# Performance work log

Hardware: AMD Instinct MI355X
Metric: run time of the kernel (lower is better)

Reference implementation:

```python
import jax, jax.numpy as jnp
import numpy as np

NBITS = 8
QMAX = 2 ** (NBITS - 1) - 1  # 127
EPS_S = 1e-8


def ste_round(x):
    # straight-through estimator round (matches HAWQ ste_round)
    return x + jax.lax.stop_gradient(jnp.round(x) - x)


def quant_act(x):
    # symmetric per-tensor 8-bit fake quantization (QuantAct)
    s = jnp.maximum(jnp.max(jnp.abs(x)) / QMAX, EPS_S)
    xq = jnp.clip(ste_round(x / s), -QMAX - 1, QMAX)
    return xq * s, s


def quant_weight_per_channel(w, axis=0):
    # symmetric per-output-channel 8-bit fake quantization (weights)
    red = tuple(i for i in range(w.ndim) if i != axis)
    s = jnp.maximum(jnp.max(jnp.abs(w), axis=red, keepdims=True) / QMAX, EPS_S)
    wq = jnp.clip(ste_round(w / s), -QMAX - 1, QMAX)
    return wq * s, s


def setup_inputs() -> dict:
    key = jax.random.key(0)
    ks = jax.random.split(key, 6)
    B, Cin, Cout, H, W = 32, 256, 128, 56, 56
    x = jax.random.normal(ks[0], (B, Cin, H, W), jnp.float32)
    bn_gamma = 1.0 + 0.1 * jax.random.normal(ks[1], (Cin,), jnp.float32)
    bn_beta = 0.1 * jax.random.normal(ks[2], (Cin,), jnp.float32)
    bn_mean = 0.1 * jax.random.normal(ks[3], (Cin,), jnp.float32)
    bn_var = jax.random.uniform(ks[4], (Cin,), jnp.float32, minval=0.5, maxval=1.5)
    conv_w = jax.random.normal(ks[5], (Cout, Cin), jnp.float32) * (1.0 / np.sqrt(Cin))
    return {"x": x, "bn_gamma": bn_gamma, "bn_beta": bn_beta,
            "bn_mean": bn_mean, "bn_var": bn_var, "conv_w": conv_w}


def reference(x, bn_gamma, bn_beta, bn_mean, bn_var, conv_w):
    bn_eps = 1e-5
    # --- QuantAct on incoming activations ---
    x, act_s = quant_act(x)
    # --- QuantBn: fold BN into per-channel scale/shift, quantize folded weight ---
    w_fold = bn_gamma * jax.lax.rsqrt(bn_var + bn_eps)        # [Cin]
    b_fold = bn_beta - bn_mean * w_fold                       # [Cin]
    wq, bn_s = quant_weight_per_channel(w_fold, axis=0)
    x = x * wq[None, :, None, None] + b_fold[None, :, None, None]
    # --- QuantAct1: requantize post-BN output (act_s * bn_s threaded) ---
    x, act_s = quant_act(x)
    # --- ReLU ---
    x = jax.nn.relu(x)
    # --- QuantConv2d: 1x1 conv, per-output-channel quantized weight ---
    cwq, conv_s = quant_weight_per_channel(conv_w, axis=0)    # [Cout, Cin]
    x = jnp.einsum('bchw,oc->bohw', x, cwq)                   # [B, Cout, H, W]
    # --- QuantAct2: requantize post-conv output ---
    x, act_s = quant_act(x)
    # --- QuantAveragePool2d(2,2): pool in integer domain, rescale back ---
    B, C, H, W = x.shape
    x_int = x / act_s
    pooled = x_int.reshape(B, C, H // 2, 2, W // 2, 2).mean(axis=(3, 5))
    x = pooled * act_s
    # --- QuantAct3 ---
    x, act_s = quant_act(x)
    return x, act_s
```

## Files before the change

kernel.cpp:

```cpp
#include <hip/hip_runtime.h>
#include <math.h>

#define QMAXF 127.0f
#define EPSF  1e-8f
#define CIN   256
#define COUT  128
#define HW    3136
#define W_    56
#define NPOOL 3211264
#define POOL_BLOCKS 1792

typedef unsigned short u16;
typedef unsigned int   u32;
typedef __attribute__((ext_vector_type(8))) short s16x8;
typedef __attribute__((ext_vector_type(4))) float f32x4;

#define WQ_OFF   8
#define BF_OFF   264
#define EMAX_OFF 520
#define EMIN_OFF 776
#define CS_OFF   1032
#define CSS2_OFF 1160
#define CWB_OFF  1288
#define LUT_OFF  17672
#define Y_OFF    50440

__device__ __forceinline__ float qclip(float v) {
    return fminf(fmaxf(v, -128.0f), 127.0f);
}
__device__ __forceinline__ u16 bf16bits(float f) {
    return (u16)(__float_as_uint(f) >> 16);
}
__device__ __forceinline__ u32 encf(float f) {
    u32 u = __float_as_uint(f);
    return (u & 0x80000000u) ? ~u : (u | 0x80000000u);
}
__device__ __forceinline__ float decf(u32 k) {
    return __uint_as_float((k & 0x80000000u) ? (k ^ 0x80000000u) : ~k);
}

__device__ __forceinline__ void block_max_atomic(float v, float* red, u32* dst) {
    #pragma unroll
    for (int off = 32; off > 0; off >>= 1) v = fmaxf(v, __shfl_xor(v, off));
    const int lane = threadIdx.x & 63, wid = threadIdx.x >> 6;
    if (lane == 0) red[wid] = v;
    __syncthreads();
    if (threadIdx.x == 0) {
        const int nw = blockDim.x >> 6;
        float m = red[0];
        for (int i = 1; i < nw; ++i) m = fmaxf(m, red[i]);
        atomicMax(dst, __float_as_uint(m));
    }
}

__global__ void k0w(const float* __restrict__ cw, float* __restrict__ ws) {
    const int t = threadIdx.x;
    if (blockIdx.x == COUT) {
        ((u32*)ws)[EMAX_OFF + t] = 0u;
        ((u32*)ws)[EMIN_OFF + t] = 0xFFFFFFFFu;
        if (t < 2) ((u32*)ws)[2 + t] = 0u;
        return;
    }
    __shared__ float red[4];
    const int o = blockIdx.x;
    const float wv = cw[o * CIN + t];
    float v = fabsf(wv);
    #pragma unroll
    for (int off = 32; off > 0; off >>= 1) v = fmaxf(v, __shfl_xor(v, off));
    if ((t & 63) == 0) red[t >> 6] = v;
    __syncthreads();
    const float mx = fmaxf(fmaxf(red[0], red[1]), fmaxf(red[2], red[3]));
    const float s = fmaxf(mx / QMAXF, EPSF);
    const float q = qclip(rintf(wv / s));
    ((u16*)(ws + CWB_OFF))[o * CIN + t] = bf16bits(q);
    if (t == 0) ws[CS_OFF + o] = s;
}

__global__ void k1_minmax(const float* __restrict__ x, float* __restrict__ ws) {
    __shared__ float red[8];
    const int row = blockIdx.x;
    const float4* xr = (const float4*)(x + (size_t)row * HW);
    float mx = -3.402823466e38f, mn = 3.402823466e38f;
    for (int i = threadIdx.x; i < HW / 4; i += 256) {
        const float4 v = xr[i];
        mx = fmaxf(mx, fmaxf(fmaxf(v.x, v.y), fmaxf(v.z, v.w)));
        mn = fminf(mn, fminf(fminf(v.x, v.y), fminf(v.z, v.w)));
    }
    #pragma unroll
    for (int off = 32; off > 0; off >>= 1) {
        mx = fmaxf(mx, __shfl_xor(mx, off));
        mn = fminf(mn, __shfl_xor(mn, off));
    }
    if ((threadIdx.x & 63) == 0) {
        red[threadIdx.x >> 6] = mx;
        red[4 + (threadIdx.x >> 6)] = mn;
    }
    __syncthreads();
    if (threadIdx.x == 0) {
        mx = fmaxf(fmaxf(red[0], red[1]), fmaxf(red[2], red[3]));
        mn = fminf(fminf(red[4], red[5]), fminf(red[6], red[7]));
        const int c = row & (CIN - 1);
        atomicMax((u32*)ws + EMAX_OFF + c, encf(mx));
        atomicMin((u32*)ws + EMIN_OFF + c, encf(mn));
    }
}

__global__ void k0b(const float* __restrict__ g, const float* __restrict__ be,
                    const float* __restrict__ mnp, const float* __restrict__ vr,
                    float* __restrict__ ws) {
    __shared__ float red[4];
    __shared__ float s1sh;
    const int t = threadIdx.x;
    const float cmax = decf(((u32*)ws)[EMAX_OFF + t]);
    const float cmin = decf(((u32*)ws)[EMIN_OFF + t]);
    float v = fmaxf(fabsf(cmax), fabsf(cmin));
    #pragma unroll
    for (int off = 32; off > 0; off >>= 1) v = fmaxf(v, __shfl_xor(v, off));
    if ((t & 63) == 0) red[t >> 6] = v;
    __syncthreads();
    if (t == 0) {
        const float m1 = fmaxf(fmaxf(red[0], red[1]), fmaxf(red[2], red[3]));
        ws[0] = m1;
        s1sh = fmaxf(m1 / QMAXF, EPSF);
    }
    __syncthreads();
    const float s1 = s1sh;
    const float wf = g[t] / sqrtf(vr[t] + 1e-5f);
    const float bf = be[t] - mnp[t] * wf;
    const float sw = fmaxf(fabsf(wf) / QMAXF, EPSF);
    const float q  = qclip(rintf(wf / sw));
    const float wqd = __fmul_rn(q, sw);
    ws[WQ_OFF + t] = wqd;
    ws[BF_OFF + t] = bf;
    const float q1h = qclip(rintf(cmax / s1));
    const float q1l = qclip(rintf(cmin / s1));
    const float xh = __fadd_rn(__fmul_rn(__fmul_rn(q1h, s1), wqd), bf);
    const float xl = __fadd_rn(__fmul_rn(__fmul_rn(q1l, s1), wqd), bf);
    float m2 = fmaxf(fabsf(xh), fabsf(xl));
    __syncthreads();
    #pragma unroll
    for (int off = 32; off > 0; off >>= 1) m2 = fmaxf(m2, __shfl_xor(m2, off));
    if ((t & 63) == 0) red[t >> 6] = m2;
    __syncthreads();
    if (t == 0) ws[1] = fmaxf(fmaxf(red[0], red[1]), fmaxf(red[2], red[3]));
}

__global__ void k0L(float* __restrict__ ws) {
    const int c = blockIdx.x;
    const int t = threadIdx.x;
    const float s1 = fmaxf(ws[0] / QMAXF, EPSF);
    const float s2 = fmaxf(ws[1] / QMAXF, EPSF);
    const float wqd = ws[WQ_OFF + c];
    const float bf  = ws[BF_OFF + c];
    const float q1f = (float)(t - 127);
    const float xd  = __fmul_rn(q1f, s1);
    const float x2  = __fadd_rn(__fmul_rn(xd, wqd), bf);
    const float q2  = qclip(rintf(x2 / s2));
    const float a   = fmaxf(q2, 0.0f);
    ((u16*)(ws + LUT_OFF))[(c << 8) + t] = bf16bits(a);
    if (c == 0 && t < COUT)
        ws[CSS2_OFF + t] = __fmul_rn(s2, ws[CS_OFF + t]);
}

__device__ __forceinline__ void stage32(u16* __restrict__ Xs, u16* __restrict__ Wt,
                                        const float* __restrict__ xr8,
                                        const s16x8* __restrict__ wreg,
                                        int t, int ck, double rinv,
                                        const u16* __restrict__ lut) {
    const int p = t & 31, kh = t >> 5;
    u32 pk[4];
    #pragma unroll
    for (int jj = 0; jj < 4; ++jj) {
        const int c0 = ck + kh * 8 + 2 * jj;
        const int q1a = (int)rintf((float)((double)xr8[2 * jj] * rinv));
        const int q1b = (int)rintf((float)((double)xr8[2 * jj + 1] * rinv));
        const u32 lo = lut[(c0 << 8) + 127 + q1a];
        const u32 hi = lut[((c0 + 1) << 8) + 127 + q1b];
        pk[jj] = lo | (hi << 16);
    }
    uint4 v; v.x = pk[0]; v.y = pk[1]; v.z = pk[2]; v.w = pk[3];
    *(uint4*)&Xs[p * 64 + (((kh + p + (p >> 3)) & 7) * 8)] = v;
    #pragma unroll
    for (int ps = 0; ps < 4; ++ps) {
        const int o = ps * 32 + (t >> 3);
        *(s16x8*)&Wt[o * 64 + ((((t & 7) + o + (o >> 3)) & 7) * 8)] = wreg[ps];
    }
}

__global__ __launch_bounds__(256) void k3_mfma(const float* __restrict__ x,
                                               float* __restrict__ ws) {
    __shared__ __align__(16) u16 Xs[32 * 64];
    __shared__ __align__(16) u16 Wt[128 * 64];
    __shared__ float Css2s[COUT];
    __shared__ float red[4];

    const int t   = threadIdx.x;
    const int b   = blockIdx.x / 98;
    const int hw0 = (blockIdx.x % 98) * 32;
    const int l   = t & 63, w = t >> 6;
    const int wc  = w * 32;

    const float s1 = fmaxf(ws[0] / QMAXF, EPSF);
    const double rinv = 1.0 / (double)s1;
    const u16* lut = (const u16*)(ws + LUT_OFF);
    const u16* cwb = (const u16*)(ws + CWB_OFF);

    if (t < COUT) Css2s[t] = ws[CSS2_OFF + t];

    const int p  = t & 31;
    const int kh = t >> 5;
    const float* xb = x + (size_t)b * CIN * HW + hw0 + p;

    float xr[32];
    #pragma unroll
    for (int it = 0; it < 4; ++it)
        #pragma unroll
        for (int j = 0; j < 8; ++j)
            xr[it * 8 + j] = xb[(it * 64 + kh * 8 + j) * HW];

    s16x8 wreg[4];
    #pragma unroll
    for (int ps = 0; ps < 4; ++ps)
        wreg[ps] = *(const s16x8*)(cwb + (ps * 32 + (t >> 3)) * CIN + (t & 7) * 8);

    f32x4 acc[2][2];
    #pragma unroll
    for (int m = 0; m < 2; ++m)
        #pragma unroll
        for (int n = 0; n < 2; ++n) acc[m][n] = (f32x4)0.0f;

    stage32(Xs, Wt, &xr[0], wreg, t, 0, rinv, lut);
    __syncthreads();

    #pragma unroll
    for (int it = 0; it < 4; ++it) {
        const int ckn = (it + 1) * 64;
        if (it < 3) {
            #pragma unroll
            for (int ps = 0; ps < 4; ++ps)
                wreg[ps] = *(const s16x8*)(cwb + (ps * 32 + (t >> 3)) * CIN + ckn + (t & 7) * 8);
        }
        #pragma unroll
        for (int ks = 0; ks < 2; ++ks) {
            const int ch = ks * 4 + (l >> 4);
            s16x8 xf[2], wfr[2];
            #pragma unroll
            for (int n = 0; n < 2; ++n) {
                const int pp = n * 16 + (l & 15);
                xf[n] = *(const s16x8*)&Xs[pp * 64 + (((ch + pp + (pp >> 3)) & 7) * 8)];
            }
            #pragma unroll
            for (int m = 0; m < 2; ++m) {
                const int o = wc + m * 16 + (l & 15);
                wfr[m] = *(const s16x8*)&Wt[o * 64 + (((ch + o + (o >> 3)) & 7) * 8)];
            }
            #pragma unroll
            for (int m = 0; m < 2; ++m)
                #pragma unroll
                for (int n = 0; n < 2; ++n)
                    acc[m][n] = __builtin_amdgcn_mfma_f32_16x16x32_bf16(
                                    wfr[m], xf[n], acc[m][n], 0, 0, 0);
        }
        if (it < 3) {
            __syncthreads();
            stage32(Xs, Wt, &xr[(it + 1) * 8], wreg, t, ckn, rinv, lut);
            __syncthreads();
        }
    }

    float mloc = 0.0f;
    #pragma unroll
    for (int m = 0; m < 2; ++m) {
        #pragma unroll
        for (int n = 0; n < 2; ++n) {
            const int pix = hw0 + n * 16 + (l & 15);
            #pragma unroll
            for (int r = 0; r < 4; ++r) {
                const int o = wc + m * 16 + (l >> 4) * 4 + r;
                const float val = __fmul_rn(acc[m][n][r], Css2s[o]);
                ws[Y_OFF + ((size_t)(b * COUT + o)) * HW + pix] = val;
                mloc = fmaxf(mloc, fabsf(val));
            }
        }
    }
    block_max_atomic(mloc, red, (u32*)ws + 2);
}

__global__ void k4_pool(float* __restrict__ ws, float* __restrict__ out) {
    __shared__ float red[4];
    const float s3 = fmaxf(ws[2] / QMAXF, EPSF);
    float mloc = 0.0f;
    const int nq2 = NPOOL / 2;
    for (int pp = blockIdx.x * 256 + threadIdx.x; pp < nq2;
         pp += POOL_BLOCKS * 256) {
        const int j2  = pp % 14;
        const int tmp = pp / 14;
        const int i   = tmp % 28;
        const int bo  = tmp / 28;
        const float* yb = ws + Y_OFF + (size_t)bo * HW + (2 * i) * W_ + 4 * j2;
        const float4 r0 = *(const float4*)yb;
        const float4 r1 = *(const float4*)(yb + W_);
        const float q00 = qclip(rintf(r0.x / s3)), q01 = qclip(rintf(r0.y / s3));
        const float q02 = qclip(rintf(r0.z / s3)), q03 = qclip(rintf(r0.w / s3));
        const float q10 = qclip(rintf(r1.x / s3)), q11 = qclip(rintf(r1.y / s3));
        const float q12 = qclip(rintf(r1.z / s3)), q13 = qclip(rintf(r1.w / s3));
        const float p0 = __fmul_rn(__fmul_rn((q00 + q01) + (q10 + q11), 0.25f), s3);
        const float p1 = __fmul_rn(__fmul_rn((q02 + q03) + (q12 + q13), 0.25f), s3);
        float2 pv; pv.x = p0; pv.y = p1;
        *(float2*)(out + (size_t)bo * 784 + i * 28 + 2 * j2) = pv;
        mloc = fmaxf(mloc, fmaxf(fabsf(p0), fabsf(p1)));
    }
    block_max_atomic(mloc, red, (u32*)ws + 3);
}

__global__ void k5_final(float* __restrict__ out, const float* __restrict__ ws) {
    const float s4 = fmaxf(ws[3] / QMAXF, EPSF);
    const int n4 = NPOOL / 4;
    for (int i = blockIdx.x * 256 + threadIdx.x; i < n4; i += 3136 * 256) {
        float4 v = *(float4*)(out + 4 * (size_t)i);
        v.x = __fmul_rn(qclip(rintf(v.x / s4)), s4);
        v.y = __fmul_rn(qclip(rintf(v.y / s4)), s4);
        v.z = __fmul_rn(qclip(rintf(v.z / s4)), s4);
        v.w = __fmul_rn(qclip(rintf(v.w / s4)), s4);
        *(float4*)(out + 4 * (size_t)i) = v;
    }
    if (blockIdx.x == 0 && threadIdx.x == 0) out[NPOOL] = s4;
}

extern "C" void kernel_launch(void* const* d_in, const int* in_sizes, int n_in,
                              void* d_out, int out_size, void* d_ws, size_t ws_size,
                              hipStream_t stream) {
    const float* x     = (const float*)d_in[0];
    const float* gamma = (const float*)d_in[1];
    const float* beta  = (const float*)d_in[2];
    const float* mean  = (const float*)d_in[3];
    const float* var   = (const float*)d_in[4];
    const float* cw    = (const float*)d_in[5];
    float* out = (float*)d_out;
    float* ws  = (float*)d_ws;

    hipLaunchKernelGGL(k0w, dim3(COUT + 1), dim3(256), 0, stream, cw, ws);
    hipLaunchKernelGGL(k1_minmax, dim3(32 * CIN), dim3(256), 0, stream, x, ws);
    hipLaunchKernelGGL(k0b, dim3(1), dim3(256), 0, stream, gamma, beta, mean, var, ws);
    hipLaunchKernelGGL(k0L, dim3(256), dim3(256), 0, stream, ws);
    hipLaunchKernelGGL(k3_mfma, dim3(3136), dim3(256), 0, stream, x, ws);
    hipLaunchKernelGGL(k4_pool, dim3(POOL_BLOCKS), dim3(256), 0, stream, ws, out);
    hipLaunchKernelGGL(k5_final, dim3(3136), dim3(256), 0, stream, out, ws);
}
```

Baseline: 116.3 us.

## Double-buffer LDS tiles in MFMA conv kernel to remove a barrier per step

Splits the staging helper into separate X and W stagers and double-buffers the Xs and Wt shared-memory tiles. The next K-chunk is staged into the alternate buffer while the current one is consumed, so each iteration needs one barrier instead of two. Weight prefetch moves to two register sets that alternate, and an empty asm statement keeps the preloaded activations in VGPRs. This roughly doubles LDS use (about 40KB) and raises register pressure, which may lower occupancy. It also still does a redundant wraparound weight load on the last staging step.

```diff
diff --git a/kernel.cpp b/kernel.cpp
--- a/kernel.cpp
+++ b/kernel.cpp
@@ -162,11 +162,10 @@
         ws[CSS2_OFF + t] = __fmul_rn(s2, ws[CS_OFF + t]);
 }
 
-__device__ __forceinline__ void stage32(u16* __restrict__ Xs, u16* __restrict__ Wt,
-                                        const float* __restrict__ xr8,
-                                        const s16x8* __restrict__ wreg,
-                                        int t, int ck, double rinv,
-                                        const u16* __restrict__ lut) {
+__device__ __forceinline__ void stageX(u16* __restrict__ Xs,
+                                       const float* __restrict__ xr8,
+                                       int t, int ck, double rinv,
+                                       const u16* __restrict__ lut) {
     const int p = t & 31, kh = t >> 5;
     u32 pk[4];
     #pragma unroll
@@ -180,6 +179,10 @@
     }
     uint4 v; v.x = pk[0]; v.y = pk[1]; v.z = pk[2]; v.w = pk[3];
     *(uint4*)&Xs[p * 64 + (((kh + p + (p >> 3)) & 7) * 8)] = v;
+}
+
+__device__ __forceinline__ void stageW(u16* __restrict__ Wt,
+                                       const s16x8* __restrict__ wreg, int t) {
     #pragma unroll
     for (int ps = 0; ps < 4; ++ps) {
         const int o = ps * 32 + (t >> 3);
@@ -189,8 +192,8 @@
 
 __global__ __launch_bounds__(256) void k3_mfma(const float* __restrict__ x,
                                                float* __restrict__ ws) {
-    __shared__ __align__(16) u16 Xs[32 * 64];
-    __shared__ __align__(16) u16 Wt[128 * 64];
+    __shared__ __align__(16) u16 Xs[2][32 * 64];
+    __shared__ __align__(16) u16 Wt[2][128 * 64];
     __shared__ float Css2s[COUT];
     __shared__ float red[4];
 
@@ -210,6 +213,7 @@
     const int p  = t & 31;
     const int kh = t >> 5;
     const float* xb = x + (size_t)b * CIN * HW + hw0 + p;
+    const u16* wsrc = cwb + ((t >> 3) & 31) * CIN + (t & 7) * 8;
 
     float xr[32];
     #pragma unroll
@@ -217,11 +221,14 @@
         #pragma unroll
         for (int j = 0; j < 8; ++j)
             xr[it * 8 + j] = xb[(it * 64 + kh * 8 + j) * HW];
-
-    s16x8 wreg[4];
+    #pragma unroll
+    for (int i = 0; i < 32; ++i)
+        asm volatile("" : "+v"(xr[i]));
+
+    s16x8 wA[4], wB[4];
     #pragma unroll
     for (int ps = 0; ps < 4; ++ps)
-        wreg[ps] = *(const s16x8*)(cwb + (ps * 32 + (t >> 3)) * CIN + (t & 7) * 8);
+        wA[ps] = *(const s16x8*)(wsrc + (ps * 32) * CIN);
 
     f32x4 acc[2][2];
     #pragma unroll
@@ -229,16 +236,29 @@
         #pragma unroll
         for (int n = 0; n < 2; ++n) acc[m][n] = (f32x4)0.0f;
 
-    stage32(Xs, Wt, &xr[0], wreg, t, 0, rinv, lut);
+    stageX(Xs[0], &xr[0], t, 0, rinv, lut);
+    stageW(Wt[0], wA, t);
+    #pragma unroll
+    for (int ps = 0; ps < 4; ++ps)
+        wB[ps] = *(const s16x8*)(wsrc + (ps * 32) * CIN + 64);
     __syncthreads();
 
     #pragma unroll
     for (int it = 0; it < 4; ++it) {
-        const int ckn = (it + 1) * 64;
+        const int cur = it & 1;
         if (it < 3) {
-            #pragma unroll
-            for (int ps = 0; ps < 4; ++ps)
-                wreg[ps] = *(const s16x8*)(cwb + (ps * 32 + (t >> 3)) * CIN + ckn + (t & 7) * 8);
+            stageX(Xs[cur ^ 1], &xr[(it + 1) * 8], t, (it + 1) * 64, rinv, lut);
+            if (it & 1) {
+                stageW(Wt[cur ^ 1], wA, t);
+                #pragma unroll
+                for (int ps = 0; ps < 4; ++ps)
+                    wB[ps] = *(const s16x8*)(wsrc + (ps * 32) * CIN + (it + 2) * 64);
+            } else {
+                stageW(Wt[cur ^ 1], wB, t);
+                #pragma unroll
+                for (int ps = 0; ps < 4; ++ps)
+                    wA[ps] = *(const s16x8*)(wsrc + (ps * 32) * CIN + ((it + 2) & 3) * 64);
+            }
         }
         #pragma unroll
         for (int ks = 0; ks < 2; ++ks) {
@@ -247,12 +267,12 @@
             #pragma unroll
             for (int n = 0; n < 2; ++n) {
                 const int pp = n * 16 + (l & 15);
-                xf[n] = *(const s16x8*)&Xs[pp * 64 + (((ch + pp + (pp >> 3)) & 7) * 8)];
+                xf[n] = *(const s16x8*)&Xs[cur][pp * 64 + (((ch + pp + (pp >> 3)) & 7) * 8)];
             }
             #pragma unroll
             for (int m = 0; m < 2; ++m) {
                 const int o = wc + m * 16 + (l & 15);
-                wfr[m] = *(const s16x8*)&Wt[o * 64 + (((ch + o + (o >> 3)) & 7) * 8)];
+                wfr[m] = *(const s16x8*)&Wt[cur][o * 64 + (((ch + o + (o >> 3)) & 7) * 8)];
             }
             #pragma unroll
             for (int m = 0; m < 2; ++m)
@@ -261,11 +281,7 @@
                     acc[m][n] = __builtin_amdgcn_mfma_f32_16x16x32_bf16(
                                     wfr[m], xf[n], acc[m][n], 0, 0, 0);
         }
-        if (it < 3) {
-            __syncthreads();
-            stage32(Xs, Wt, &xr[(it + 1) * 8], wreg, t, ckn, rinv, lut);
-            __syncthreads();
-        }
+        __syncthreads();
     }
 
     float mloc = 0.0f;
```

After: 118.8 us. 2.2% more time.

## Replace per-channel BN requant lookup table with inline arithmetic and drop LUT kernel

Applied to the files above, without the earlier changes.

Removes the k0L kernel that built a 256x256 bf16 lookup table for the BN+requant+ReLU step, and instead computes the requantized activation inline in the GEMM staging using per-channel scale/shift cached in shared memory. The CSS2 product is moved into k0b, saving one kernel launch. Division by scale in pool and final kernels is replaced by double-precision multiply by reciprocal. This trades scattered global LUT gathers and a launch for extra ALU work (including double-precision conversions) in the staging path.

```diff
diff --git a/kernel.cpp b/kernel.cpp
--- a/kernel.cpp
+++ b/kernel.cpp
@@ -22,7 +22,6 @@
 #define CS_OFF   1032
 #define CSS2_OFF 1160
 #define CWB_OFF  1288
-#define LUT_OFF  17672
 #define Y_OFF    50440
 
 __device__ __forceinline__ float qclip(float v) {
@@ -109,7 +108,7 @@
                     const float* __restrict__ mnp, const float* __restrict__ vr,
                     float* __restrict__ ws) {
     __shared__ float red[4];
-    __shared__ float s1sh;
+    __shared__ float s1sh, s2sh;
     const int t = threadIdx.x;
     const float cmax = decf(((u32*)ws)[EMAX_OFF + t]);
     const float cmin = decf(((u32*)ws)[EMIN_OFF + t]);
@@ -142,44 +141,43 @@
     for (int off = 32; off > 0; off >>= 1) m2 = fmaxf(m2, __shfl_xor(m2, off));
     if ((t & 63) == 0) red[t >> 6] = m2;
     __syncthreads();
-    if (t == 0) ws[1] = fmaxf(fmaxf(red[0], red[1]), fmaxf(red[2], red[3]));
-}
-
-__global__ void k0L(float* __restrict__ ws) {
-    const int c = blockIdx.x;
-    const int t = threadIdx.x;
-    const float s1 = fmaxf(ws[0] / QMAXF, EPSF);
-    const float s2 = fmaxf(ws[1] / QMAXF, EPSF);
-    const float wqd = ws[WQ_OFF + c];
-    const float bf  = ws[BF_OFF + c];
-    const float q1f = (float)(t - 127);
-    const float xd  = __fmul_rn(q1f, s1);
-    const float x2  = __fadd_rn(__fmul_rn(xd, wqd), bf);
-    const float q2  = qclip(rintf(x2 / s2));
-    const float a   = fmaxf(q2, 0.0f);
-    ((u16*)(ws + LUT_OFF))[(c << 8) + t] = bf16bits(a);
-    if (c == 0 && t < COUT)
-        ws[CSS2_OFF + t] = __fmul_rn(s2, ws[CS_OFF + t]);
-}
-
-__device__ __forceinline__ void stage32(u16* __restrict__ Xs, u16* __restrict__ Wt,
-                                        const float* __restrict__ xr8,
-                                        const s16x8* __restrict__ wreg,
-                                        int t, int ck, double rinv,
-                                        const u16* __restrict__ lut) {
+    if (t == 0) {
+        const float m2f = fmaxf(fmaxf(red[0], red[1]), fmaxf(red[2], red[3]));
+        ws[1] = m2f;
+        s2sh = fmaxf(m2f / QMAXF, EPSF);
+    }
+    __syncthreads();
+    if (t < COUT) ws[CSS2_OFF + t] = __fmul_rn(s2sh, ws[CS_OFF + t]);
+}
+
+__device__ __forceinline__ void stageX(u16* __restrict__ Xs,
+                                       const float* __restrict__ xr8,
+                                       const float2* __restrict__ wqbf,
+                                       int t, int ck, float s1,
+                                       double rinv1, double rinv2) {
     const int p = t & 31, kh = t >> 5;
     u32 pk[4];
     #pragma unroll
     for (int jj = 0; jj < 4; ++jj) {
         const int c0 = ck + kh * 8 + 2 * jj;
-        const int q1a = (int)rintf((float)((double)xr8[2 * jj] * rinv));
-        const int q1b = (int)rintf((float)((double)xr8[2 * jj + 1] * rinv));
-        const u32 lo = lut[(c0 << 8) + 127 + q1a];
-        const u32 hi = lut[((c0 + 1) << 8) + 127 + q1b];
-        pk[jj] = lo | (hi << 16);
+        float a2[2];
+        #pragma unroll
+        for (int u = 0; u < 2; ++u) {
+            const float2 wb = wqbf[c0 + u];
+            const float q1 = rintf((float)((double)xr8[2 * jj + u] * rinv1));
+            const float xd = __fmul_rn(q1, s1);
+            const float x2 = __fadd_rn(__fmul_rn(xd, wb.x), wb.y);
+            const float q2 = rintf((float)((double)x2 * rinv2));
+            a2[u] = fminf(fmaxf(q2, 0.0f), 127.0f);
+        }
+        pk[jj] = (__float_as_uint(a2[0]) >> 16) | (__float_as_uint(a2[1]) & 0xFFFF0000u);
     }
     uint4 v; v.x = pk[0]; v.y = pk[1]; v.z = pk[2]; v.w = pk[3];
     *(uint4*)&Xs[p * 64 + (((kh + p + (p >> 3)) & 7) * 8)] = v;
+}
+
+__device__ __forceinline__ void stageW(u16* __restrict__ Wt,
+                                       const s16x8* __restrict__ wreg, int t) {
     #pragma unroll
     for (int ps = 0; ps < 4; ++ps) {
         const int o = ps * 32 + (t >> 3);
@@ -191,6 +189,7 @@
                                                float* __restrict__ ws) {
     __shared__ __align__(16) u16 Xs[32 * 64];
     __shared__ __align__(16) u16 Wt[128 * 64];
+    __shared__ float2 wqbfs[CIN];
     __shared__ float Css2s[COUT];
     __shared__ float red[4];
 
@@ -201,15 +200,19 @@
     const int wc  = w * 32;
 
     const float s1 = fmaxf(ws[0] / QMAXF, EPSF);
-    const double rinv = 1.0 / (double)s1;
-    const u16* lut = (const u16*)(ws + LUT_OFF);
+    const float s2 = fmaxf(ws[1] / QMAXF, EPSF);
+    const double rinv1 = 1.0 / (double)s1;
+    const double rinv2 = 1.0 / (double)s2;
     const u16* cwb = (const u16*)(ws + CWB_OFF);
 
+    float2 wb0; wb0.x = ws[WQ_OFF + t]; wb0.y = ws[BF_OFF + t];
+    wqbfs[t] = wb0;
     if (t < COUT) Css2s[t] = ws[CSS2_OFF + t];
 
     const int p  = t & 31;
     const int kh = t >> 5;
     const float* xb = x + (size_t)b * CIN * HW + hw0 + p;
+    const u16* wsrc = cwb + ((t >> 3) & 31) * CIN + (t & 7) * 8;
 
     float xr[32];
     #pragma unroll
@@ -221,7 +224,7 @@
     s16x8 wreg[4];
     #pragma unroll
     for (int ps = 0; ps < 4; ++ps)
-        wreg[ps] = *(const s16x8*)(cwb + (ps * 32 + (t >> 3)) * CIN + (t & 7) * 8);
+        wreg[ps] = *(const s16x8*)(wsrc + (ps * 32) * CIN);
 
     f32x4 acc[2][2];
     #pragma unroll
@@ -229,7 +232,9 @@
         #pragma unroll
         for (int n = 0; n < 2; ++n) acc[m][n] = (f32x4)0.0f;
 
-    stage32(Xs, Wt, &xr[0], wreg, t, 0, rinv, lut);
+    __syncthreads();
+    stageX(Xs, &xr[0], wqbfs, t, 0, s1, rinv1, rinv2);
+    stageW(Wt, wreg, t);
     __syncthreads();
 
     #pragma unroll
@@ -238,7 +243,7 @@
         if (it < 3) {
             #pragma unroll
             for (int ps = 0; ps < 4; ++ps)
-                wreg[ps] = *(const s16x8*)(cwb + (ps * 32 + (t >> 3)) * CIN + ckn + (t & 7) * 8);
+                wreg[ps] = *(const s16x8*)(wsrc + (ps * 32) * CIN + ckn);
         }
         #pragma unroll
         for (int ks = 0; ks < 2; ++ks) {
@@ -263,7 +268,8 @@
         }
         if (it < 3) {
             __syncthreads();
-            stage32(Xs, Wt, &xr[(it + 1) * 8], wreg, t, ckn, rinv, lut);
+            stageX(Xs, &xr[(it + 1) * 8], wqbfs, t, ckn, s1, rinv1, rinv2);
+            stageW(Wt, wreg, t);
             __syncthreads();
         }
     }
@@ -289,6 +295,7 @@
 __global__ void k4_pool(float* __restrict__ ws, float* __restrict__ out) {
     __shared__ float red[4];
     const float s3 = fmaxf(ws[2] / QMAXF, EPSF);
+    const double rinv3 = 1.0 / (double)s3;
     float mloc = 0.0f;
     const int nq2 = NPOOL / 2;
     for (int pp = blockIdx.x * 256 + threadIdx.x; pp < nq2;
@@ -300,10 +307,14 @@
         const float* yb = ws + Y_OFF + (size_t)bo * HW + (2 * i) * W_ + 4 * j2;
         const float4 r0 = *(const float4*)yb;
         const float4 r1 = *(const float4*)(yb + W_);
-        const float q00 = qclip(rintf(r0.x / s3)), q01 = qclip(rintf(r0.y / s3));
-        const float q02 = qclip(rintf(r0.z / s3)), q03 = qclip(rintf(r0.w / s3));
-        const float q10 = qclip(rintf(r1.x / s3)), q11 = qclip(rintf(r1.y / s3));
-        const float q12 = qclip(rintf(r1.z / s3)), q13 = qclip(rintf(r1.w / s3));
+        const float q00 = qclip(rintf((float)((double)r0.x * rinv3)));
+        const float q01 = qclip(rintf((float)((double)r0.y * rinv3)));
+        const float q02 = qclip(rintf((float)((double)r0.z * rinv3)));
+        const float q03 = qclip(rintf((float)((double)r0.w * rinv3)));
+        const float q10 = qclip(rintf((float)((double)r1.x * rinv3)));
+        const float q11 = qclip(rintf((float)((double)r1.y * rinv3)));
+        const float q12 = qclip(rintf((float)((double)r1.z * rinv3)));
+        const float q13 = qclip(rintf((float)((double)r1.w * rinv3)));
         const float p0 = __fmul_rn(__fmul_rn((q00 + q01) + (q10 + q11), 0.25f), s3);
         const float p1 = __fmul_rn(__fmul_rn((q02 + q03) + (q12 + q13), 0.25f), s3);
         float2 pv; pv.x = p0; pv.y = p1;
@@ -315,13 +326,14 @@
 
 __global__ void k5_final(float* __restrict__ out, const float* __restrict__ ws) {
     const float s4 = fmaxf(ws[3] / QMAXF, EPSF);
+    const double rinv4 = 1.0 / (double)s4;
     const int n4 = NPOOL / 4;
     for (int i = blockIdx.x * 256 + threadIdx.x; i < n4; i += 3136 * 256) {
         float4 v = *(float4*)(out + 4 * (size_t)i);
-        v.x = __fmul_rn(qclip(rintf(v.x / s4)), s4);
-        v.y = __fmul_rn(qclip(rintf(v.y / s4)), s4);
-        v.z = __fmul_rn(qclip(rintf(v.z / s4)), s4);
-        v.w = __fmul_rn(qclip(rintf(v.w / s4)), s4);
+        v.x = __fmul_rn(qclip(rintf((float)((double)v.x * rinv4))), s4);
+        v.y = __fmul_rn(qclip(rintf((float)((double)v.y * rinv4))), s4);
+        v.z = __fmul_rn(qclip(rintf((float)((double)v.z * rinv4))), s4);
+        v.w = __fmul_rn(qclip(rintf((float)((double)v.w * rinv4))), s4);
         *(float4*)(out + 4 * (size_t)i) = v;
     }
     if (blockIdx.x == 0 && threadIdx.x == 0) out[NPOOL] = s4;
@@ -342,7 +354,6 @@
     hipLaunchKernelGGL(k0w, dim3(COUT + 1), dim3(256), 0, stream, cw, ws);
     hipLaunchKernelGGL(k1_minmax, dim3(32 * CIN), dim3(256), 0, stream, x, ws);
     hipLaunchKernelGGL(k0b, dim3(1), dim3(256), 0, stream, gamma, beta, mean, var, ws);
-    hipLaunchKernelGGL(k0L, dim3(256), dim3(256), 0, stream, ws);
     hipLaunchKernelGGL(k3_mfma, dim3(3136), dim3(256), 0, stream, x, ws);
     hipLaunchKernelGGL(k4_pool, dim3(POOL_BLOCKS), dim3(256), 0, stream, ws, out);
     hipLaunchKernelGGL(k5_final, dim3(3136), dim3(256), 0, stream, out, ws);
```

Result: slower. 243.9 us (+109.8%).

## Stage full-K activation tile once and read conv weights directly from global

Applied to the files above, without the earlier changes.

The MFMA conv kernel now quantizes and writes the whole 256-channel activation tile for its 32 pixels into shared memory in one pass, with a single barrier, instead of four staged chunks each bracketed by two barriers. The conv weights are no longer staged through shared memory; each wave loads its MFMA weight fragments straight from global (likely cached) memory. This cuts synchronization and shared-memory write traffic, but raises shared memory per block for activations and relies on cache hits for the repeated weight loads.

```diff
diff --git a/kernel.cpp b/kernel.cpp
--- a/kernel.cpp
+++ b/kernel.cpp
@@ -162,35 +162,9 @@
         ws[CSS2_OFF + t] = __fmul_rn(s2, ws[CS_OFF + t]);
 }
 
-__device__ __forceinline__ void stage32(u16* __restrict__ Xs, u16* __restrict__ Wt,
-                                        const float* __restrict__ xr8,
-                                        const s16x8* __restrict__ wreg,
-                                        int t, int ck, double rinv,
-                                        const u16* __restrict__ lut) {
-    const int p = t & 31, kh = t >> 5;
-    u32 pk[4];
-    #pragma unroll
-    for (int jj = 0; jj < 4; ++jj) {
-        const int c0 = ck + kh * 8 + 2 * jj;
-        const int q1a = (int)rintf((float)((double)xr8[2 * jj] * rinv));
-        const int q1b = (int)rintf((float)((double)xr8[2 * jj + 1] * rinv));
-        const u32 lo = lut[(c0 << 8) + 127 + q1a];
-        const u32 hi = lut[((c0 + 1) << 8) + 127 + q1b];
-        pk[jj] = lo | (hi << 16);
-    }
-    uint4 v; v.x = pk[0]; v.y = pk[1]; v.z = pk[2]; v.w = pk[3];
-    *(uint4*)&Xs[p * 64 + (((kh + p + (p >> 3)) & 7) * 8)] = v;
-    #pragma unroll
-    for (int ps = 0; ps < 4; ++ps) {
-        const int o = ps * 32 + (t >> 3);
-        *(s16x8*)&Wt[o * 64 + ((((t & 7) + o + (o >> 3)) & 7) * 8)] = wreg[ps];
-    }
-}
-
 __global__ __launch_bounds__(256) void k3_mfma(const float* __restrict__ x,
                                                float* __restrict__ ws) {
-    __shared__ __align__(16) u16 Xs[32 * 64];
-    __shared__ __align__(16) u16 Wt[128 * 64];
+    __shared__ __align__(16) u16 Xs[32 * 256];
     __shared__ float Css2s[COUT];
     __shared__ float red[4];
 
@@ -201,7 +175,7 @@
     const int wc  = w * 32;
 
     const float s1 = fmaxf(ws[0] / QMAXF, EPSF);
-    const double rinv = 1.0 / (double)s1;
+    const double rinv1 = 1.0 / (double)s1;
     const u16* lut = (const u16*)(ws + LUT_OFF);
     const u16* cwb = (const u16*)(ws + CWB_OFF);
 
@@ -210,18 +184,28 @@
     const int p  = t & 31;
     const int kh = t >> 5;
     const float* xb = x + (size_t)b * CIN * HW + hw0 + p;
-
-    float xr[32];
-    #pragma unroll
-    for (int it = 0; it < 4; ++it)
+    const int sw8 = ((kh + p + (p >> 3)) & 7) * 8;
+
+    #pragma unroll
+    for (int g = 0; g < 4; ++g) {
+        float xv[8];
         #pragma unroll
         for (int j = 0; j < 8; ++j)
-            xr[it * 8 + j] = xb[(it * 64 + kh * 8 + j) * HW];
-
-    s16x8 wreg[4];
-    #pragma unroll
-    for (int ps = 0; ps < 4; ++ps)
-        wreg[ps] = *(const s16x8*)(cwb + (ps * 32 + (t >> 3)) * CIN + (t & 7) * 8);
+            xv[j] = xb[(g * 64 + kh * 8 + j) * HW];
+        u32 pk[4];
+        #pragma unroll
+        for (int jj = 0; jj < 4; ++jj) {
+            const int c0 = g * 64 + kh * 8 + 2 * jj;
+            const u32 qa = (u32)((int)rintf((float)((double)xv[2 * jj]     * rinv1)) + 127);
+            const u32 qb = (u32)((int)rintf((float)((double)xv[2 * jj + 1] * rinv1)) + 127);
+            const u32 lo = lut[(c0 << 8) + qa];
+            const u32 hi = lut[((c0 + 1) << 8) + qb];
+            pk[jj] = lo | (hi << 16);
+        }
+        uint4 v; v.x = pk[0]; v.y = pk[1]; v.z = pk[2]; v.w = pk[3];
+        *(uint4*)&Xs[p * 256 + g * 64 + sw8] = v;
+    }
+    __syncthreads();
 
     f32x4 acc[2][2];
     #pragma unroll
@@ -229,31 +213,25 @@
         #pragma unroll
         for (int n = 0; n < 2; ++n) acc[m][n] = (f32x4)0.0f;
 
-    stage32(Xs, Wt, &xr[0], wreg, t, 0, rinv, lut);
-    __syncthreads();
+    const int lm = l & 15, lh = l >> 4;
+    const u16* wbase0 = cwb + (wc + lm) * CIN + lh * 8;
+    const u16* wbase1 = cwb + (wc + 16 + lm) * CIN + lh * 8;
 
     #pragma unroll
     for (int it = 0; it < 4; ++it) {
-        const int ckn = (it + 1) * 64;
-        if (it < 3) {
-            #pragma unroll
-            for (int ps = 0; ps < 4; ++ps)
-                wreg[ps] = *(const s16x8*)(cwb + (ps * 32 + (t >> 3)) * CIN + ckn + (t & 7) * 8);
-        }
         #pragma unroll
         for (int ks = 0; ks < 2; ++ks) {
-            const int ch = ks * 4 + (l >> 4);
+            const int ch = ks * 4 + lh;
+            const int ko = it * 64 + ks * 32;
             s16x8 xf[2], wfr[2];
             #pragma unroll
             for (int n = 0; n < 2; ++n) {
-                const int pp = n * 16 + (l & 15);
-                xf[n] = *(const s16x8*)&Xs[pp * 64 + (((ch + pp + (pp >> 3)) & 7) * 8)];
+                const int pp = n * 16 + lm;
+                xf[n] = *(const s16x8*)&Xs[pp * 256 + it * 64 +
+                                           (((ch + pp + (pp >> 3)) & 7) * 8)];
             }
-            #pragma unroll
-            for (int m = 0; m < 2; ++m) {
-                const int o = wc + m * 16 + (l & 15);
-                wfr[m] = *(const s16x8*)&Wt[o * 64 + (((ch + o + (o >> 3)) & 7) * 8)];
-            }
+            wfr[0] = *(const s16x8*)(wbase0 + ko);
+            wfr[1] = *(const s16x8*)(wbase1 + ko);
             #pragma unroll
             for (int m = 0; m < 2; ++m)
                 #pragma unroll
@@ -261,11 +239,6 @@
                     acc[m][n] = __builtin_amdgcn_mfma_f32_16x16x32_bf16(
                                     wfr[m], xf[n], acc[m][n], 0, 0, 0);
         }
-        if (it < 3) {
-            __syncthreads();
-            stage32(Xs, Wt, &xr[(it + 1) * 8], wreg, t, ckn, rinv, lut);
-            __syncthreads();
-        }
     }
 
     float mloc = 0.0f;
@@ -273,10 +246,10 @@
     for (int m = 0; m < 2; ++m) {
         #pragma unroll
         for (int n = 0; n < 2; ++n) {
-            const int pix = hw0 + n * 16 + (l & 15);
+            const int pix = hw0 + n * 16 + lm;
             #pragma unroll
             for (int r = 0; r < 4; ++r) {
-                const int o = wc + m * 16 + (l >> 4) * 4 + r;
+                const int o = wc + m * 16 + lh * 4 + r;
                 const float val = __fmul_rn(acc[m][n][r], Css2s[o]);
                 ws[Y_OFF + ((size_t)(b * COUT + o)) * HW + pix] = val;
                 mloc = fmaxf(mloc, fabsf(val));
```

Measured after the change: 121.6 us. 4.6% more time.
